# Performance work log

Measured on AMD Instinct MI355X. Metric: run time of the kernel, lower is better.

## Reference

```python
import jax, jax.numpy as jnp
import numpy as np

N = 50000        # nodes
E = 800000       # edges (before self-loops)
F_IN = 128       # input features
HID = 32         # per-head hidden channels
H1 = 4           # heads of conv1
H2 = 8           # heads of conv2
NEG_SLOPE = 0.2  # PyG GATConv LeakyReLU slope
E_DEC = 100000   # pos/neg decode edges each


def setup_inputs() -> dict:
    key = jax.random.key(0)
    ks = jax.random.split(key, 12)
    s = 0.1
    return {
        "x": jax.random.normal(ks[0], (N, F_IN), jnp.float32),
        "edge_index": jax.random.randint(ks[1], (2, E), 0, N, dtype=jnp.int32),
        "pos_edge_index": jax.random.randint(ks[2], (2, E_DEC), 0, N, dtype=jnp.int32),
        "neg_edge_index": jax.random.randint(ks[3], (2, E_DEC), 0, N, dtype=jnp.int32),
        "W1": jax.random.normal(ks[4], (F_IN, H1 * HID), jnp.float32) * s,
        "a_src1": jax.random.normal(ks[5], (H1, HID), jnp.float32) * s,
        "a_dst1": jax.random.normal(ks[6], (H1, HID), jnp.float32) * s,
        "b1": jax.random.normal(ks[7], (H1 * HID,), jnp.float32) * s,
        "W2": jax.random.normal(ks[8], (H1 * HID, H2 * HID), jnp.float32) * s,
        "a_src2": jax.random.normal(ks[9], (H2, HID), jnp.float32) * s,
        "a_dst2": jax.random.normal(ks[10], (H2, HID), jnp.float32) * s,
        "b2": jax.random.normal(ks[11], (H2 * HID,), jnp.float32) * s,
    }


def _segment_softmax(e, seg, n):
    # softmax over edges grouped by destination node; max is detached (cancels analytically)
    m = jax.lax.stop_gradient(jax.ops.segment_max(e, seg, num_segments=n))
    ex = jnp.exp(e - m[seg])
    denom = jax.ops.segment_sum(ex, seg, num_segments=n)
    return ex / (denom[seg] + 1e-16)


def _gat_conv(x, src, dst, W, a_src, a_dst, b, heads, out_ch):
    n = x.shape[0]
    h = (x @ W).reshape(n, heads, out_ch)             # [N,H,C]
    al_s = (h * a_src[None]).sum(-1)                  # [N,H]
    al_d = (h * a_dst[None]).sum(-1)                  # [N,H]
    e = al_s[src] + al_d[dst]                         # [E,H] edge logits
    e = jnp.where(e > 0, e, NEG_SLOPE * e)            # LeakyReLU
    alpha = _segment_softmax(e, dst, n)               # [E,H]
    msg = h[src] * alpha[:, :, None]                  # [E,H,C]
    out = jax.ops.segment_sum(msg, dst, num_segments=n)  # [N,H,C]
    return out.reshape(n, heads * out_ch) + b


def reference(x, edge_index, pos_edge_index, neg_edge_index,
              W1, a_src1, a_dst1, b1, W2, a_src2, a_dst2, b2):
    n = x.shape[0]
    loops = jnp.arange(n, dtype=edge_index.dtype)     # PyG add_self_loops=True
    src = jnp.concatenate([edge_index[0], loops])
    dst = jnp.concatenate([edge_index[1], loops])
    # encode
    z = jax.nn.relu(_gat_conv(x, src, dst, W1, a_src1, a_dst1, b1, H1, HID))
    z = _gat_conv(z, src, dst, W2, a_src2, a_dst2, b2, H2, HID)
    # decode
    ei = jnp.concatenate([pos_edge_index, neg_edge_index], axis=1)
    logits = (z[ei[0]] * z[ei[1]]).sum(-1)            # [2*E_DEC]
    return logits
```

## Files before the change

kernel.cpp:

```cpp
#include <hip/hip_runtime.h>
#include <hip/hip_bf16.h>

#define NN 50000
#define EE 800000
#define ET (EE + NN)
#define F_IN 128
#define HID 32
#define H1 4
#define H2 8
#define E_DEC 100000
#define NEG_SLOPE 0.2f

typedef __attribute__((ext_vector_type(8))) short short8;
typedef __attribute__((ext_vector_type(4))) float floatx4;

__device__ __forceinline__ unsigned short f2b(float f) {
    __hip_bfloat16 h = __float2bfloat16(f);
    return *reinterpret_cast<unsigned short*>(&h);
}
__device__ __forceinline__ float b2f(unsigned short u) {
    return __uint_as_float(((unsigned int)u) << 16);
}

__global__ void fillint_k(int* __restrict__ p, int n) {
    int i = blockIdx.x * blockDim.x + threadIdx.x;
    if (i < n) p[i] = 0;
}

__global__ void hist_k(const int* __restrict__ ei, int* __restrict__ counts) {
    int e = blockIdx.x * blockDim.x + threadIdx.x;
    if (e >= ET) return;
    int d = (e < EE) ? ei[EE + e] : e - EE;
    atomicAdd(&counts[d], 1);
}

__global__ void scan1_k(const int* __restrict__ counts, int* __restrict__ bsum) {
    __shared__ int sh[256];
    int t = threadIdx.x;
    int i = blockIdx.x * 256 + t;
    sh[t] = (i < NN) ? counts[i] : 0;
    __syncthreads();
    for (int off = 128; off > 0; off >>= 1) {
        if (t < off) sh[t] += sh[t + off];
        __syncthreads();
    }
    if (t == 0) bsum[blockIdx.x] = sh[0];
}

__global__ void scan2_k(int* __restrict__ bsum, int nb, int* __restrict__ start) {
    __shared__ int sh[256];
    int t = threadIdx.x;
    int v = (t < nb) ? bsum[t] : 0;
    sh[t] = v;
    __syncthreads();
    for (int off = 1; off < 256; off <<= 1) {
        int u = (t >= off) ? sh[t - off] : 0;
        __syncthreads();
        sh[t] += u;
        __syncthreads();
    }
    if (t < nb) bsum[t] = sh[t] - v;
    if (t == 0) start[NN] = ET;
}

__global__ void scan3_k(const int* __restrict__ counts, const int* __restrict__ bsum,
                        int* __restrict__ start, int* __restrict__ cursor) {
    __shared__ int sh[256];
    int t = threadIdx.x;
    int i = blockIdx.x * 256 + t;
    int c = (i < NN) ? counts[i] : 0;
    sh[t] = c;
    __syncthreads();
    for (int off = 1; off < 256; off <<= 1) {
        int u = (t >= off) ? sh[t - off] : 0;
        __syncthreads();
        sh[t] += u;
        __syncthreads();
    }
    int excl = sh[t] - c + bsum[blockIdx.x];
    if (i < NN) {
        start[i] = excl;
        cursor[i] = excl;
    }
}

__global__ void scatter_k(const int* __restrict__ ei, int* __restrict__ cursor,
                          int* __restrict__ csr) {
    int e = blockIdx.x * blockDim.x + threadIdx.x;
    if (e >= ET) return;
    int s, d;
    if (e < EE) { s = ei[e]; d = ei[EE + e]; } else { s = d = e - EE; }
    int slot = atomicAdd(&cursor[d], 1);
    csr[slot] = s;
}

template <int OUT>
__global__ void packW_k(const float* __restrict__ W, unsigned short* __restrict__ Wp) {
    const int total = (OUT / 16) * 4 * 64;
    int id = blockIdx.x * 256 + threadIdx.x;
    if (id >= total) return;
    const int col = ((id >> 8) << 4) + (id & 15);
    const int k0 = ((id >> 6) & 3) * 32 + ((id >> 4) & 3) * 8;
    ushort4 lo, hi;
    lo.x = f2b(W[(k0 + 0) * OUT + col]);
    lo.y = f2b(W[(k0 + 1) * OUT + col]);
    lo.z = f2b(W[(k0 + 2) * OUT + col]);
    lo.w = f2b(W[(k0 + 3) * OUT + col]);
    hi.x = f2b(W[(k0 + 4) * OUT + col]);
    hi.y = f2b(W[(k0 + 5) * OUT + col]);
    hi.z = f2b(W[(k0 + 6) * OUT + col]);
    hi.w = f2b(W[(k0 + 7) * OUT + col]);
    ((ushort4*)Wp)[id * 2] = lo;
    ((ushort4*)Wp)[id * 2 + 1] = hi;
}

template <int OUT, int H, int CT, bool F32IN>
__global__ void mfma_gemm_k(const void* __restrict__ Xin,
                            const unsigned short* __restrict__ Wp,
                            const float* __restrict__ a_src, const float* __restrict__ a_dst,
                            unsigned short* __restrict__ Hout,
                            float* __restrict__ als, float* __restrict__ ald) {
    const int wave = threadIdx.x >> 6;
    const int lane = threadIdx.x & 63;
    const int quad = lane >> 4;
    const int rl = lane & 15;
    const int r0 = blockIdx.x * 64;
    floatx4 acc[4][CT];
#pragma unroll
    for (int rt = 0; rt < 4; ++rt)
#pragma unroll
        for (int ct = 0; ct < CT; ++ct) acc[rt][ct] = {0.f, 0.f, 0.f, 0.f};

#pragma unroll
    for (int ks = 0; ks < 4; ++ks) {
        short8 a[4];
#pragma unroll
        for (int rt = 0; rt < 4; ++rt) {
            int row = r0 + rt * 16 + rl;
            row = row < NN ? row : NN - 1;
            if (F32IN) {
                const float4* xp =
                    (const float4*)((const float*)Xin + (long long)row * 128 + ks * 32 + quad * 8);
                const float4 v0 = xp[0];
                const float4 v1 = xp[1];
                short8 t;
                t[0] = (short)f2b(v0.x);
                t[1] = (short)f2b(v0.y);
                t[2] = (short)f2b(v0.z);
                t[3] = (short)f2b(v0.w);
                t[4] = (short)f2b(v1.x);
                t[5] = (short)f2b(v1.y);
                t[6] = (short)f2b(v1.z);
                t[7] = (short)f2b(v1.w);
                a[rt] = t;
            } else {
                a[rt] = *(const short8*)((const unsigned short*)Xin +
                                         (long long)row * 128 + ks * 32 + quad * 8);
            }
        }
#pragma unroll
        for (int ct = 0; ct < CT; ++ct) {
            const int ctg = wave * CT + ct;
            const short8 b = *(const short8*)(Wp + (((ctg * 4 + ks) * 64 + lane) << 3));
#pragma unroll
            for (int rt = 0; rt < 4; ++rt)
                acc[rt][ct] = __builtin_amdgcn_mfma_f32_16x16x32_bf16(a[rt], b, acc[rt][ct], 0, 0, 0);
        }
    }
#pragma unroll
    for (int rt = 0; rt < 4; ++rt) {
        const int rowbase = r0 + rt * 16 + quad * 4;
#pragma unroll
        for (int ct = 0; ct < CT; ++ct) {
            const int col = (wave * CT + ct) * 16 + rl;
#pragma unroll
            for (int r = 0; r < 4; ++r) {
                const int row = rowbase + r;
                if (row < NN) Hout[(long long)row * OUT + col] = f2b(acc[rt][ct][r]);
            }
        }
    }
    float asv[CT], adv[CT];
#pragma unroll
    for (int ct = 0; ct < CT; ++ct) {
        const int col = (wave * CT + ct) * 16 + rl;
        asv[ct] = a_src[col];
        adv[ct] = a_dst[col];
    }
#pragma unroll
    for (int rt = 0; rt < 4; ++rt) {
#pragma unroll
        for (int r = 0; r < 4; ++r) {
            const int row = r0 + rt * 16 + quad * 4 + r;
            float ps[CT / 2], pd[CT / 2];
#pragma unroll
            for (int hh = 0; hh < CT / 2; ++hh) {
                ps[hh] = acc[rt][2 * hh][r] * asv[2 * hh] + acc[rt][2 * hh + 1][r] * asv[2 * hh + 1];
                pd[hh] = acc[rt][2 * hh][r] * adv[2 * hh] + acc[rt][2 * hh + 1][r] * adv[2 * hh + 1];
#pragma unroll
                for (int m = 8; m >= 1; m >>= 1) {
                    ps[hh] += __shfl_xor(ps[hh], m, 64);
                    pd[hh] += __shfl_xor(pd[hh], m, 64);
                }
            }
            if (rl == 0 && row < NN) {
#pragma unroll
                for (int hh = 0; hh < CT / 2; ++hh) {
                    const int hd = wave * (CT / 2) + hh;
                    als[row * H + hd] = ps[hh];
                    ald[row * H + hd] = pd[hh];
                }
            }
        }
    }
}

template <int OUT, int H, bool RELU>
__global__ void gather_k(const int* __restrict__ start, const int* __restrict__ csr,
                         const float* __restrict__ als, const float* __restrict__ ald,
                         const unsigned short* __restrict__ Hin,
                         const float* __restrict__ bias, unsigned short* __restrict__ outp) {
    constexpr int LPR = OUT / 4;
    constexpr int EPW = 64 / LPR;
    const int d = blockIdx.x;
    const int lane = threadIdx.x;
    const int cl = lane & (LPR - 1);
    const int slot = lane >> (LPR == 64 ? 6 : 5);
    const int hd = cl >> 3;
    const int beg = start[d], end = start[d + 1];
    const float aldd = ald[d * H + hd];
    float a0 = 0.f, a1 = 0.f, a2 = 0.f, a3 = 0.f, den = 0.f;
    int i = beg + slot;
    for (; i + 3 * EPW < end; i += 4 * EPW) {
        const int s0 = csr[i], s1 = csr[i + EPW], s2 = csr[i + 2 * EPW], s3 = csr[i + 3 * EPW];
        float l0 = als[s0 * H + hd] + aldd;
        float l1 = als[s1 * H + hd] + aldd;
        float l2 = als[s2 * H + hd] + aldd;
        float l3 = als[s3 * H + hd] + aldd;
        const ushort4 h0 = *(const ushort4*)(Hin + (long long)s0 * OUT + cl * 4);
        const ushort4 h1 = *(const ushort4*)(Hin + (long long)s1 * OUT + cl * 4);
        const ushort4 h2 = *(const ushort4*)(Hin + (long long)s2 * OUT + cl * 4);
        const ushort4 h3 = *(const ushort4*)(Hin + (long long)s3 * OUT + cl * 4);
        l0 = l0 > 0.f ? l0 : NEG_SLOPE * l0;
        l1 = l1 > 0.f ? l1 : NEG_SLOPE * l1;
        l2 = l2 > 0.f ? l2 : NEG_SLOPE * l2;
        l3 = l3 > 0.f ? l3 : NEG_SLOPE * l3;
        const float w0 = __expf(l0), w1 = __expf(l1), w2 = __expf(l2), w3 = __expf(l3);
        den += (w0 + w1) + (w2 + w3);
        a0 += w0 * b2f(h0.x) + w1 * b2f(h1.x) + w2 * b2f(h2.x) + w3 * b2f(h3.x);
        a1 += w0 * b2f(h0.y) + w1 * b2f(h1.y) + w2 * b2f(h2.y) + w3 * b2f(h3.y);
        a2 += w0 * b2f(h0.z) + w1 * b2f(h1.z) + w2 * b2f(h2.z) + w3 * b2f(h3.z);
        a3 += w0 * b2f(h0.w) + w1 * b2f(h1.w) + w2 * b2f(h2.w) + w3 * b2f(h3.w);
    }
    for (; i < end; i += EPW) {
        const int s = csr[i];
        float lg = als[s * H + hd] + aldd;
        lg = lg > 0.f ? lg : NEG_SLOPE * lg;
        const float w = __expf(lg);
        const ushort4 hv = *(const ushort4*)(Hin + (long long)s * OUT + cl * 4);
        den += w;
        a0 += w * b2f(hv.x);
        a1 += w * b2f(hv.y);
        a2 += w * b2f(hv.z);
        a3 += w * b2f(hv.w);
    }
    if (EPW == 2) {
        a0 += __shfl_xor(a0, 32, 64);
        a1 += __shfl_xor(a1, 32, 64);
        a2 += __shfl_xor(a2, 32, 64);
        a3 += __shfl_xor(a3, 32, 64);
        den += __shfl_xor(den, 32, 64);
    }
    if (lane < LPR) {
        const float inv = 1.f / (den + 1e-16f);
        const int c0 = cl * 4;
        float v0 = a0 * inv + bias[c0];
        float v1 = a1 * inv + bias[c0 + 1];
        float v2 = a2 * inv + bias[c0 + 2];
        float v3 = a3 * inv + bias[c0 + 3];
        if (RELU) {
            v0 = v0 > 0.f ? v0 : 0.f;
            v1 = v1 > 0.f ? v1 : 0.f;
            v2 = v2 > 0.f ? v2 : 0.f;
            v3 = v3 > 0.f ? v3 : 0.f;
        }
        ushort4 o;
        o.x = f2b(v0);
        o.y = f2b(v1);
        o.z = f2b(v2);
        o.w = f2b(v3);
        *(ushort4*)(outp + (long long)d * OUT + c0) = o;
    }
}

__global__ void decode_k(const int* __restrict__ pei, const int* __restrict__ nei,
                         const unsigned short* __restrict__ z2, float* __restrict__ out) {
    const int w = threadIdx.x >> 6, lane = threadIdx.x & 63;
    const int idx = blockIdx.x * 4 + w;
    if (idx >= 2 * E_DEC) return;
    int a, b;
    if (idx < E_DEC) {
        a = pei[idx];
        b = pei[E_DEC + idx];
    } else {
        const int j = idx - E_DEC;
        a = nei[j];
        b = nei[E_DEC + j];
    }
    const ushort4 ua = *(const ushort4*)(z2 + (long long)a * 256 + lane * 4);
    const ushort4 ub = *(const ushort4*)(z2 + (long long)b * 256 + lane * 4);
    float s = b2f(ua.x) * b2f(ub.x) + b2f(ua.y) * b2f(ub.y) +
              b2f(ua.z) * b2f(ub.z) + b2f(ua.w) * b2f(ub.w);
#pragma unroll
    for (int m = 32; m >= 1; m >>= 1) s += __shfl_xor(s, m, 64);
    if (lane == 0) out[idx] = s;
}

extern "C" void kernel_launch(void* const* d_in, const int* in_sizes, int n_in,
                              void* d_out, int out_size, void* d_ws, size_t ws_size,
                              hipStream_t stream) {
    const float* x = (const float*)d_in[0];
    const int* ei = (const int*)d_in[1];
    const int* pei = (const int*)d_in[2];
    const int* nei = (const int*)d_in[3];
    const float* W1 = (const float*)d_in[4];
    const float* as1 = (const float*)d_in[5];
    const float* ad1 = (const float*)d_in[6];
    const float* b1 = (const float*)d_in[7];
    const float* W2 = (const float*)d_in[8];
    const float* as2 = (const float*)d_in[9];
    const float* ad2 = (const float*)d_in[10];
    const float* b2 = (const float*)d_in[11];
    float* out = (float*)d_out;

    unsigned short* h1 = (unsigned short*)d_ws;
    unsigned short* h2 = h1 + (long long)NN * 128;
    unsigned short* z2 = h2 + (long long)NN * 256;
    unsigned short* z1 = z2 + (long long)NN * 256;
    unsigned short* wp1 = z1 + (long long)NN * 128;
    unsigned short* wp2 = wp1 + 128 * 128;
    float* als1 = (float*)(wp2 + 128 * 256);
    float* ald1 = als1 + NN * H1;
    float* als2 = ald1 + NN * H1;
    float* ald2 = als2 + NN * H2;
    int* counts = (int*)(ald2 + NN * H2);
    int* start = counts + NN;
    int* cursor = start + NN + 1;
    int* bsum = cursor + NN;
    int* csr = bsum + 256;

    const int NB = (NN + 255) / 256;

    fillint_k<<<NB, 256, 0, stream>>>(counts, NN);
    hist_k<<<(ET + 255) / 256, 256, 0, stream>>>(ei, counts);
    scan1_k<<<NB, 256, 0, stream>>>(counts, bsum);
    scan2_k<<<1, 256, 0, stream>>>(bsum, NB, start);
    scan3_k<<<NB, 256, 0, stream>>>(counts, bsum, start, cursor);
    scatter_k<<<(ET + 255) / 256, 256, 0, stream>>>(ei, cursor, csr);

    packW_k<128><<<(2048 + 255) / 256, 256, 0, stream>>>(W1, wp1);
    packW_k<256><<<(4096 + 255) / 256, 256, 0, stream>>>(W2, wp2);

    mfma_gemm_k<128, H1, 2, true><<<(NN + 63) / 64, 256, 0, stream>>>(
        x, wp1, as1, ad1, h1, als1, ald1);
    gather_k<128, H1, true><<<NN, 64, 0, stream>>>(start, csr, als1, ald1, h1, b1, z1);

    mfma_gemm_k<256, H2, 4, false><<<(NN + 63) / 64, 256, 0, stream>>>(
        z1, wp2, as2, ad2, h2, als2, ald2);
    gather_k<256, H2, false><<<NN, 64, 0, stream>>>(start, csr, als2, ald2, h2, b2, z2);

    decode_k<<<(2 * E_DEC + 3) / 4, 256, 0, stream>>>(pei, nei, z2, out);
}
```

Before: 380.4 us.

## Streamline CSR build, unroll gather by eight, batch decode per wave

Replaces the three-kernel scan with a single-block 1024-thread chunked scan and drops the histogram pass over self-loops by initialising counts to one. Histogram and scatter now read edge indices as int4 and handle four edges per thread. The gather loop gains an 8-way unrolled body so more independent loads are in flight per step, and decode handles two edges per wave. The single-block scan serialises about 49 chunks on one CU, which may cost more than the launches it removes.

```diff
diff --git a/kernel.cpp b/kernel.cpp
--- a/kernel.cpp
+++ b/kernel.cpp
@@ -22,76 +22,70 @@
     return __uint_as_float(((unsigned int)u) << 16);
 }
 
-__global__ void fillint_k(int* __restrict__ p, int n) {
+__global__ void fillone_k(int* __restrict__ p, int n) {
     int i = blockIdx.x * blockDim.x + threadIdx.x;
-    if (i < n) p[i] = 0;
+    if (i < n) p[i] = 1;
 }
 
 __global__ void hist_k(const int* __restrict__ ei, int* __restrict__ counts) {
-    int e = blockIdx.x * blockDim.x + threadIdx.x;
-    if (e >= ET) return;
-    int d = (e < EE) ? ei[EE + e] : e - EE;
-    atomicAdd(&counts[d], 1);
-}
-
-__global__ void scan1_k(const int* __restrict__ counts, int* __restrict__ bsum) {
-    __shared__ int sh[256];
-    int t = threadIdx.x;
-    int i = blockIdx.x * 256 + t;
-    sh[t] = (i < NN) ? counts[i] : 0;
+    int t = blockIdx.x * blockDim.x + threadIdx.x;
+    if (t >= EE / 4) return;
+    const int4 d4 = ((const int4*)(ei + EE))[t];
+    atomicAdd(&counts[d4.x], 1);
+    atomicAdd(&counts[d4.y], 1);
+    atomicAdd(&counts[d4.z], 1);
+    atomicAdd(&counts[d4.w], 1);
+}
+
+__global__ void scanall_k(const int* __restrict__ counts, int* __restrict__ start,
+                          int* __restrict__ cursor) {
+    __shared__ int sh[1024];
+    __shared__ int base;
+    const int t = threadIdx.x;
+    if (t == 0) base = 0;
     __syncthreads();
-    for (int off = 128; off > 0; off >>= 1) {
-        if (t < off) sh[t] += sh[t + off];
+    for (int c0 = 0; c0 < NN; c0 += 1024) {
+        const int i = c0 + t;
+        const int c = (i < NN) ? counts[i] : 0;
+        sh[t] = c;
         __syncthreads();
-    }
-    if (t == 0) bsum[blockIdx.x] = sh[0];
-}
-
-__global__ void scan2_k(int* __restrict__ bsum, int nb, int* __restrict__ start) {
-    __shared__ int sh[256];
-    int t = threadIdx.x;
-    int v = (t < nb) ? bsum[t] : 0;
-    sh[t] = v;
-    __syncthreads();
-    for (int off = 1; off < 256; off <<= 1) {
-        int u = (t >= off) ? sh[t - off] : 0;
+        for (int off = 1; off < 1024; off <<= 1) {
+            const int u = (t >= off) ? sh[t - off] : 0;
+            __syncthreads();
+            sh[t] += u;
+            __syncthreads();
+        }
+        const int excl = base + sh[t] - c;
+        if (i < NN) {
+            start[i] = excl;
+            cursor[i] = excl;
+        }
         __syncthreads();
-        sh[t] += u;
+        if (t == 1023) base += sh[1023];
         __syncthreads();
     }
-    if (t < nb) bsum[t] = sh[t] - v;
     if (t == 0) start[NN] = ET;
-}
-
-__global__ void scan3_k(const int* __restrict__ counts, const int* __restrict__ bsum,
-                        int* __restrict__ start, int* __restrict__ cursor) {
-    __shared__ int sh[256];
-    int t = threadIdx.x;
-    int i = blockIdx.x * 256 + t;
-    int c = (i < NN) ? counts[i] : 0;
-    sh[t] = c;
-    __syncthreads();
-    for (int off = 1; off < 256; off <<= 1) {
-        int u = (t >= off) ? sh[t - off] : 0;
-        __syncthreads();
-        sh[t] += u;
-        __syncthreads();
-    }
-    int excl = sh[t] - c + bsum[blockIdx.x];
-    if (i < NN) {
-        start[i] = excl;
-        cursor[i] = excl;
-    }
 }
 
 __global__ void scatter_k(const int* __restrict__ ei, int* __restrict__ cursor,
                           int* __restrict__ csr) {
-    int e = blockIdx.x * blockDim.x + threadIdx.x;
-    if (e >= ET) return;
-    int s, d;
-    if (e < EE) { s = ei[e]; d = ei[EE + e]; } else { s = d = e - EE; }
-    int slot = atomicAdd(&cursor[d], 1);
-    csr[slot] = s;
+    const int NT_E = EE / 4;
+    const int t = blockIdx.x * blockDim.x + threadIdx.x;
+    if (t < NT_E) {
+        const int4 s4 = ((const int4*)ei)[t];
+        const int4 d4 = ((const int4*)(ei + EE))[t];
+        csr[atomicAdd(&cursor[d4.x], 1)] = s4.x;
+        csr[atomicAdd(&cursor[d4.y], 1)] = s4.y;
+        csr[atomicAdd(&cursor[d4.z], 1)] = s4.z;
+        csr[atomicAdd(&cursor[d4.w], 1)] = s4.w;
+    } else {
+        const int j = (t - NT_E) * 4;
+#pragma unroll
+        for (int k = 0; k < 4; ++k) {
+            const int n = j + k;
+            if (n < NN) csr[atomicAdd(&cursor[n], 1)] = n;
+        }
+    }
 }
 
 template <int OUT>
@@ -143,16 +137,16 @@
                     (const float4*)((const float*)Xin + (long long)row * 128 + ks * 32 + quad * 8);
                 const float4 v0 = xp[0];
                 const float4 v1 = xp[1];
-                short8 t;
-                t[0] = (short)f2b(v0.x);
-                t[1] = (short)f2b(v0.y);
-                t[2] = (short)f2b(v0.z);
-                t[3] = (short)f2b(v0.w);
-                t[4] = (short)f2b(v1.x);
-                t[5] = (short)f2b(v1.y);
-                t[6] = (short)f2b(v1.z);
-                t[7] = (short)f2b(v1.w);
-                a[rt] = t;
+                short8 tt;
+                tt[0] = (short)f2b(v0.x);
+                tt[1] = (short)f2b(v0.y);
+                tt[2] = (short)f2b(v0.z);
+                tt[3] = (short)f2b(v0.w);
+                tt[4] = (short)f2b(v1.x);
+                tt[5] = (short)f2b(v1.y);
+                tt[6] = (short)f2b(v1.z);
+                tt[7] = (short)f2b(v1.w);
+                a[rt] = tt;
             } else {
                 a[rt] = *(const short8*)((const unsigned short*)Xin +
                                          (long long)row * 128 + ks * 32 + quad * 8);
@@ -231,26 +225,47 @@
     const float aldd = ald[d * H + hd];
     float a0 = 0.f, a1 = 0.f, a2 = 0.f, a3 = 0.f, den = 0.f;
     int i = beg + slot;
+    for (; i + 7 * EPW < end; i += 8 * EPW) {
+        int s[8];
+        float l[8];
+        ushort4 hv[8];
+#pragma unroll
+        for (int k = 0; k < 8; ++k) s[k] = csr[i + k * EPW];
+#pragma unroll
+        for (int k = 0; k < 8; ++k) l[k] = als[s[k] * H + hd] + aldd;
+#pragma unroll
+        for (int k = 0; k < 8; ++k) hv[k] = *(const ushort4*)(Hin + (long long)s[k] * OUT + cl * 4);
+#pragma unroll
+        for (int k = 0; k < 8; ++k) {
+            float lg = l[k] > 0.f ? l[k] : NEG_SLOPE * l[k];
+            const float w = __expf(lg);
+            den += w;
+            a0 += w * b2f(hv[k].x);
+            a1 += w * b2f(hv[k].y);
+            a2 += w * b2f(hv[k].z);
+            a3 += w * b2f(hv[k].w);
+        }
+    }
     for (; i + 3 * EPW < end; i += 4 * EPW) {
-        const int s0 = csr[i], s1 = csr[i + EPW], s2 = csr[i + 2 * EPW], s3 = csr[i + 3 * EPW];
-        float l0 = als[s0 * H + hd] + aldd;
-        float l1 = als[s1 * H + hd] + aldd;
-        float l2 = als[s2 * H + hd] + aldd;
-        float l3 = als[s3 * H + hd] + aldd;
-        const ushort4 h0 = *(const ushort4*)(Hin + (long long)s0 * OUT + cl * 4);
-        const ushort4 h1 = *(const ushort4*)(Hin + (long long)s1 * OUT + cl * 4);
-        const ushort4 h2 = *(const ushort4*)(Hin + (long long)s2 * OUT + cl * 4);
-        const ushort4 h3 = *(const ushort4*)(Hin + (long long)s3 * OUT + cl * 4);
-        l0 = l0 > 0.f ? l0 : NEG_SLOPE * l0;
-        l1 = l1 > 0.f ? l1 : NEG_SLOPE * l1;
-        l2 = l2 > 0.f ? l2 : NEG_SLOPE * l2;
-        l3 = l3 > 0.f ? l3 : NEG_SLOPE * l3;
-        const float w0 = __expf(l0), w1 = __expf(l1), w2 = __expf(l2), w3 = __expf(l3);
-        den += (w0 + w1) + (w2 + w3);
-        a0 += w0 * b2f(h0.x) + w1 * b2f(h1.x) + w2 * b2f(h2.x) + w3 * b2f(h3.x);
-        a1 += w0 * b2f(h0.y) + w1 * b2f(h1.y) + w2 * b2f(h2.y) + w3 * b2f(h3.y);
-        a2 += w0 * b2f(h0.z) + w1 * b2f(h1.z) + w2 * b2f(h2.z) + w3 * b2f(h3.z);
-        a3 += w0 * b2f(h0.w) + w1 * b2f(h1.w) + w2 * b2f(h2.w) + w3 * b2f(h3.w);
+        int s[4];
+        float l[4];
+        ushort4 hv[4];
+#pragma unroll
+        for (int k = 0; k < 4; ++k) s[k] = csr[i + k * EPW];
+#pragma unroll
+        for (int k = 0; k < 4; ++k) l[k] = als[s[k] * H + hd] + aldd;
+#pragma unroll
+        for (int k = 0; k < 4; ++k) hv[k] = *(const ushort4*)(Hin + (long long)s[k] * OUT + cl * 4);
+#pragma unroll
+        for (int k = 0; k < 4; ++k) {
+            float lg = l[k] > 0.f ? l[k] : NEG_SLOPE * l[k];
+            const float w = __expf(lg);
+            den += w;
+            a0 += w * b2f(hv[k].x);
+            a1 += w * b2f(hv[k].y);
+            a2 += w * b2f(hv[k].z);
+            a3 += w * b2f(hv[k].w);
+        }
     }
     for (; i < end; i += EPW) {
         const int s = csr[i];
@@ -295,25 +310,42 @@
 
 __global__ void decode_k(const int* __restrict__ pei, const int* __restrict__ nei,
                          const unsigned short* __restrict__ z2, float* __restrict__ out) {
-    const int w = threadIdx.x >> 6, lane = threadIdx.x & 63;
-    const int idx = blockIdx.x * 4 + w;
-    if (idx >= 2 * E_DEC) return;
-    int a, b;
-    if (idx < E_DEC) {
-        a = pei[idx];
-        b = pei[E_DEC + idx];
-    } else {
-        const int j = idx - E_DEC;
-        a = nei[j];
-        b = nei[E_DEC + j];
-    }
-    const ushort4 ua = *(const ushort4*)(z2 + (long long)a * 256 + lane * 4);
-    const ushort4 ub = *(const ushort4*)(z2 + (long long)b * 256 + lane * 4);
-    float s = b2f(ua.x) * b2f(ub.x) + b2f(ua.y) * b2f(ub.y) +
-              b2f(ua.z) * b2f(ub.z) + b2f(ua.w) * b2f(ub.w);
-#pragma unroll
-    for (int m = 32; m >= 1; m >>= 1) s += __shfl_xor(s, m, 64);
-    if (lane == 0) out[idx] = s;
+    const int wave = threadIdx.x >> 6, lane = threadIdx.x & 63;
+    const int base = blockIdx.x * 8 + wave * 2;
+    int av[2], bv[2];
+    bool ok[2];
+#pragma unroll
+    for (int k = 0; k < 2; ++k) {
+        const int idx = base + k;
+        ok[k] = idx < 2 * E_DEC;
+        int a = 0, b = 0;
+        if (ok[k]) {
+            if (idx < E_DEC) {
+                a = pei[idx];
+                b = pei[E_DEC + idx];
+            } else {
+                const int j = idx - E_DEC;
+                a = nei[j];
+                b = nei[E_DEC + j];
+            }
+        }
+        av[k] = a;
+        bv[k] = b;
+    }
+    ushort4 ua[2], ub[2];
+#pragma unroll
+    for (int k = 0; k < 2; ++k) {
+        ua[k] = *(const ushort4*)(z2 + (long long)av[k] * 256 + lane * 4);
+        ub[k] = *(const ushort4*)(z2 + (long long)bv[k] * 256 + lane * 4);
+    }
+#pragma unroll
+    for (int k = 0; k < 2; ++k) {
+        float s = b2f(ua[k].x) * b2f(ub[k].x) + b2f(ua[k].y) * b2f(ub[k].y) +
+                  b2f(ua[k].z) * b2f(ub[k].z) + b2f(ua[k].w) * b2f(ub[k].w);
+#pragma unroll
+        for (int m = 32; m >= 1; m >>= 1) s += __shfl_xor(s, m, 64);
+        if (lane == 0 && ok[k]) out[base + k] = s;
+    }
 }
 
 extern "C" void kernel_launch(void* const* d_in, const int* in_sizes, int n_in,
@@ -346,17 +378,17 @@
     int* counts = (int*)(ald2 + NN * H2);
     int* start = counts + NN;
     int* cursor = start + NN + 1;
-    int* bsum = cursor + NN;
-    int* csr = bsum + 256;
+    int* csr = cursor + NN;
 
     const int NB = (NN + 255) / 256;
 
-    fillint_k<<<NB, 256, 0, stream>>>(counts, NN);
-    hist_k<<<(ET + 255) / 256, 256, 0, stream>>>(ei, counts);
-    scan1_k<<<NB, 256, 0, stream>>>(counts, bsum);
-    scan2_k<<<1, 256, 0, stream>>>(bsum, NB, start);
-    scan3_k<<<NB, 256, 0, stream>>>(counts, bsum, start, cursor);
-    scatter_k<<<(ET + 255) / 256, 256, 0, stream>>>(ei, cursor, csr);
+    fillone_k<<<NB, 256, 0, stream>>>(counts, NN);
+    hist_k<<<(EE / 4 + 255) / 256, 256, 0, stream>>>(ei, counts);
+    scanall_k<<<1, 1024, 0, stream>>>(counts, start, cursor);
+    {
+        const int nt = EE / 4 + (NN + 3) / 4;
+        scatter_k<<<(nt + 255) / 256, 256, 0, stream>>>(ei, cursor, csr);
+    }
 
     packW_k<128><<<(2048 + 255) / 256, 256, 0, stream>>>(W1, wp1);
     packW_k<256><<<(4096 + 255) / 256, 256, 0, stream>>>(W2, wp2);
@@ -369,5 +401,5 @@
         z1, wp2, as2, ad2, h2, als2, ald2);
     gather_k<256, H2, false><<<NN, 64, 0, stream>>>(start, csr, als2, ald2, h2, b2, z2);
 
-    decode_k<<<(2 * E_DEC + 3) / 4, 256, 0, stream>>>(pei, nei, z2, out);
-}
+    decode_k<<<(2 * E_DEC + 7) / 8, 256, 0, stream>>>(pei, nei, z2, out);
+}
```

New measurement: 446.5 us. +17.4%, slower.
